# Performance work log

Hardware: AMD Instinct MI355X
Metric: run time of the kernel (lower is better)

Reference implementation:

```python
import jax, jax.numpy as jnp
import numpy as np

ALPHA = 1.0

def setup_inputs() -> dict:
    key = jax.random.key(0)
    kz, kc = jax.random.split(key)
    N, K, D = 65536, 256, 256
    z = jax.random.normal(kz, (N, D), dtype=jnp.float32)
    centroids = jax.random.normal(kc, (K, D), dtype=jnp.float32)
    return {"z": z, "centroids": centroids}

def reference(z, centroids):
    # squared euclidean distances (N, K) via expansion; same math as
    # sum((z[:,None,:]-c)**2, -1) without the (N,K,D) intermediate
    z2 = jnp.sum(z * z, axis=1, keepdims=True)            # (N, 1)
    c2 = jnp.sum(centroids * centroids, axis=1)           # (K,)
    sse = jnp.maximum(z2 + c2[None, :] - 2.0 * (z @ centroids.T), 0.0)
    # Student-t kernel
    q = (1.0 + sse / ALPHA) ** (-(ALPHA + 1.0) / 2.0)
    q = q / jnp.sum(q, axis=1, keepdims=True)             # row normalize
    # target distribution p
    sf = q * q / jnp.sum(q, axis=0, keepdims=True)        # col normalize of q^2
    p = sf / jnp.sum(sf, axis=1, keepdims=True)           # row normalize
    return (p, q)
```

## Files before the change

### kernel.cpp

```cpp
#include <hip/hip_runtime.h>
#include <stdint.h>

#define N_ROWS 65536
#define K_CENT 256
#define D_DIM  256

typedef __attribute__((ext_vector_type(8))) short bf16x8;
typedef __attribute__((ext_vector_type(4))) float f32x4;

__device__ __forceinline__ float bf2f(unsigned short u) {
    union { unsigned int i; float f; } v;
    v.i = ((unsigned int)u) << 16;
    return v.f;
}

__device__ __forceinline__ unsigned short f2bf(float f) {
    union { float f; unsigned int i; } v;
    v.f = f;
    unsigned int r = (v.i + 0x7FFFu + ((v.i >> 16) & 1u)) >> 16;
    return (unsigned short)r;
}

__global__ void c2_kernel(const float* __restrict__ cent,
                          float* __restrict__ c2,
                          unsigned short* __restrict__ cent_bf) {
    int row  = blockIdx.x;
    int lane = threadIdx.x;
    const float4 v = *(const float4*)(cent + (size_t)row * D_DIM + lane * 4);
    unsigned short b0 = f2bf(v.x), b1 = f2bf(v.y), b2 = f2bf(v.z), b3 = f2bf(v.w);
    ushort4 bv; bv.x = b0; bv.y = b1; bv.z = b2; bv.w = b3;
    *(ushort4*)(cent_bf + (size_t)row * D_DIM + lane * 4) = bv;
    float f0 = bf2f(b0), f1 = bf2f(b1), f2 = bf2f(b2), f3 = bf2f(b3);
    float s = f0 * f0 + f1 * f1 + f2 * f2 + f3 * f3;
    #pragma unroll
    for (int off = 32; off >= 1; off >>= 1) s += __shfl_xor(s, off, 64);
    if (lane == 0) c2[row] = s;
}

__global__ void pass1_kernel(const float* __restrict__ z,
                             const unsigned short* __restrict__ cent_bf,
                             const float* __restrict__ c2,
                             float* __restrict__ s_col,
                             float* __restrict__ q_out) {
    __shared__ float col_lds[4][K_CENT];

    const int tid  = threadIdx.x;
    const int wave = tid >> 6;
    const int lane = tid & 63;
    const int m15  = lane & 15;
    const int quad = lane >> 4;
    const int row0 = blockIdx.x * 64 + wave * 16;

    f32x4 acc[16];
    #pragma unroll
    for (int t = 0; t < 16; ++t) acc[t] = (f32x4){0.f, 0.f, 0.f, 0.f};

    const float*          za = z + (size_t)(row0 + m15) * D_DIM + quad * 8;
    const unsigned short* ba = cent_bf + (size_t)m15 * D_DIM + quad * 8;

    float z2p = 0.0f;
    for (int ks = 0; ks < D_DIM; ks += 32) {
        float4 a0 = *(const float4*)(za + ks);
        float4 a1 = *(const float4*)(za + ks + 4);
        bf16x8 afrag;
        unsigned short ub[8];
        ub[0] = f2bf(a0.x); ub[1] = f2bf(a0.y); ub[2] = f2bf(a0.z); ub[3] = f2bf(a0.w);
        ub[4] = f2bf(a1.x); ub[5] = f2bf(a1.y); ub[6] = f2bf(a1.z); ub[7] = f2bf(a1.w);
        #pragma unroll
        for (int j = 0; j < 8; ++j) {
            afrag[j] = (short)ub[j];
            float f = bf2f(ub[j]);
            z2p += f * f;
        }
        #pragma unroll
        for (int t = 0; t < 16; ++t) {
            bf16x8 bfrag = *(const bf16x8*)(ba + (size_t)t * 16 * D_DIM + ks);
            acc[t] = __builtin_amdgcn_mfma_f32_16x16x32_bf16(afrag, bfrag, acc[t], 0, 0, 0);
        }
    }

    z2p += __shfl_xor(z2p, 16, 64);
    z2p += __shfl_xor(z2p, 32, 64);
    float z2r[4];
    #pragma unroll
    for (int r = 0; r < 4; ++r) z2r[r] = __shfl(z2p, quad * 4 + r, 64);

    float rowsum[4] = {0.f, 0.f, 0.f, 0.f};
    #pragma unroll
    for (int t = 0; t < 16; ++t) {
        float c2v = c2[t * 16 + m15];
        #pragma unroll
        for (int r = 0; r < 4; ++r) {
            float sse = z2r[r] + c2v - 2.0f * acc[t][r];
            sse = fmaxf(sse, 0.0f);
            float u = 1.0f / (1.0f + sse);
            acc[t][r] = u;
            rowsum[r] += u;
        }
    }
    #pragma unroll
    for (int r = 0; r < 4; ++r) {
        float v = rowsum[r];
        v += __shfl_xor(v, 1, 64);
        v += __shfl_xor(v, 2, 64);
        v += __shfl_xor(v, 4, 64);
        v += __shfl_xor(v, 8, 64);
        rowsum[r] = 1.0f / v;
    }

    float colp[16];
    #pragma unroll
    for (int t = 0; t < 16; ++t) {
        float cp = 0.0f;
        #pragma unroll
        for (int r = 0; r < 4; ++r) {
            float qv = acc[t][r] * rowsum[r];
            cp += qv;
            q_out[(size_t)(row0 + quad * 4 + r) * K_CENT + t * 16 + m15] = qv;
        }
        cp += __shfl_xor(cp, 16, 64);
        cp += __shfl_xor(cp, 32, 64);
        colp[t] = cp;
    }
    if (quad == 0) {
        #pragma unroll
        for (int t = 0; t < 16; ++t) col_lds[wave][t * 16 + lane] = colp[t];
    }
    __syncthreads();
    float sp = col_lds[0][tid] + col_lds[1][tid] + col_lds[2][tid] + col_lds[3][tid];
    atomicAdd(&s_col[tid], sp);
}

__global__ void pass2_kernel(const float* __restrict__ q,
                             const float* __restrict__ s_col,
                             float* __restrict__ p) {
    const int tid  = threadIdx.x;
    const int lane = tid & 63;
    const int wave = tid >> 6;
    const int wid  = blockIdx.x * 4 + wave;

    const float4 sv = *(const float4*)(s_col + lane * 4);
    const float is0 = 1.0f / sv.x, is1 = 1.0f / sv.y,
                is2 = 1.0f / sv.z, is3 = 1.0f / sv.w;

    for (int it = 0; it < 32; ++it) {
        const int row = wid * 32 + it;
        const float4 qv = *(const float4*)(q + (size_t)row * K_CENT + lane * 4);
        float sf0 = qv.x * qv.x * is0, sf1 = qv.y * qv.y * is1;
        float sf2 = qv.z * qv.z * is2, sf3 = qv.w * qv.w * is3;
        float part = sf0 + sf1 + sf2 + sf3;
        #pragma unroll
        for (int off = 32; off >= 1; off >>= 1) part += __shfl_xor(part, off, 64);
        const float rinv = 1.0f / part;
        float4 ov;
        ov.x = sf0 * rinv; ov.y = sf1 * rinv;
        ov.z = sf2 * rinv; ov.w = sf3 * rinv;
        *(float4*)(p + (size_t)row * K_CENT + lane * 4) = ov;
    }
}

extern "C" void kernel_launch(void* const* d_in, const int* in_sizes, int n_in,
                              void* d_out, int out_size, void* d_ws, size_t ws_size,
                              hipStream_t stream) {
    const float* z    = (const float*)d_in[0];
    const float* cent = (const float*)d_in[1];
    float* p_out = (float*)d_out;
    float* q_out = p_out + (size_t)N_ROWS * K_CENT;

    float* c2    = (float*)d_ws;
    float* s_col = c2 + K_CENT;
    unsigned short* cent_bf = (unsigned short*)(s_col + K_CENT);

    hipMemsetAsync(s_col, 0, K_CENT * sizeof(float), stream);
    c2_kernel<<<K_CENT, 64, 0, stream>>>(cent, c2, cent_bf);
    pass1_kernel<<<N_ROWS / 64, 256, 0, stream>>>(z, cent_bf, c2, s_col, q_out);
    pass2_kernel<<<N_ROWS / (4 * 32), 256, 0, stream>>>(q_out, s_col, p_out);
}
```

Baseline: 256.6 us.

## Stage swizzled bf16 centroids in LDS and preload A fragments; widen pass2 grid

Pass1 loads all A fragments (z rows converted to bf16) into registers first. It then streams the bf16 centroids through a 32KB LDS buffer in four 64-row chunks, using an XOR swizzle written by c2_kernel so the B-fragment reads avoid bank conflicts. Previously every wave read B fragments straight from global/L2. Pass2 now handles 8 rows per wave with all loads issued up front, giving four times as many blocks and more memory-level parallelism. The costs are extra syncthreads, LDS use that limits occupancy, and higher register pressure.

Measured after the change: 230.4 us. 1.11x faster.

```diff
diff --git a/kernel.cpp b/kernel.cpp
--- a/kernel.cpp
+++ b/kernel.cpp
@@ -29,7 +29,9 @@
     const float4 v = *(const float4*)(cent + (size_t)row * D_DIM + lane * 4);
     unsigned short b0 = f2bf(v.x), b1 = f2bf(v.y), b2 = f2bf(v.z), b3 = f2bf(v.w);
     ushort4 bv; bv.x = b0; bv.y = b1; bv.z = b2; bv.w = b3;
-    *(ushort4*)(cent_bf + (size_t)row * D_DIM + lane * 4) = bv;
+    int blk = lane >> 1;
+    int pos = row * D_DIM + (((blk ^ (row & 7)) << 3) | ((lane & 1) << 2));
+    *(ushort4*)(cent_bf + pos) = bv;
     float f0 = bf2f(b0), f1 = bf2f(b1), f2 = bf2f(b2), f3 = bf2f(b3);
     float s = f0 * f0 + f1 * f1 + f2 * f2 + f3 * f3;
     #pragma unroll
@@ -37,11 +39,13 @@
     if (lane == 0) c2[row] = s;
 }
 
-__global__ void pass1_kernel(const float* __restrict__ z,
-                             const unsigned short* __restrict__ cent_bf,
-                             const float* __restrict__ c2,
-                             float* __restrict__ s_col,
-                             float* __restrict__ q_out) {
+__global__ __launch_bounds__(256, 4) void pass1_kernel(
+        const float* __restrict__ z,
+        const unsigned short* __restrict__ cent_bf,
+        const float* __restrict__ c2,
+        float* __restrict__ s_col,
+        float* __restrict__ q_out) {
+    __shared__ __align__(16) unsigned short bstage[64 * D_DIM];
     __shared__ float col_lds[4][K_CENT];
 
     const int tid  = threadIdx.x;
@@ -51,39 +55,55 @@
     const int quad = lane >> 4;
     const int row0 = blockIdx.x * 64 + wave * 16;
 
-    f32x4 acc[16];
-    #pragma unroll
-    for (int t = 0; t < 16; ++t) acc[t] = (f32x4){0.f, 0.f, 0.f, 0.f};
-
-    const float*          za = z + (size_t)(row0 + m15) * D_DIM + quad * 8;
-    const unsigned short* ba = cent_bf + (size_t)m15 * D_DIM + quad * 8;
-
+    const float* za = z + (size_t)(row0 + m15) * D_DIM + quad * 8;
+    bf16x8 afrag[8];
     float z2p = 0.0f;
-    for (int ks = 0; ks < D_DIM; ks += 32) {
-        float4 a0 = *(const float4*)(za + ks);
-        float4 a1 = *(const float4*)(za + ks + 4);
-        bf16x8 afrag;
-        unsigned short ub[8];
-        ub[0] = f2bf(a0.x); ub[1] = f2bf(a0.y); ub[2] = f2bf(a0.z); ub[3] = f2bf(a0.w);
-        ub[4] = f2bf(a1.x); ub[5] = f2bf(a1.y); ub[6] = f2bf(a1.z); ub[7] = f2bf(a1.w);
+    #pragma unroll
+    for (int ks = 0; ks < 8; ++ks) {
+        float4 a0 = *(const float4*)(za + ks * 32);
+        float4 a1 = *(const float4*)(za + ks * 32 + 4);
+        float av[8] = {a0.x, a0.y, a0.z, a0.w, a1.x, a1.y, a1.z, a1.w};
         #pragma unroll
         for (int j = 0; j < 8; ++j) {
-            afrag[j] = (short)ub[j];
-            float f = bf2f(ub[j]);
+            unsigned short ub = f2bf(av[j]);
+            afrag[ks][j] = (short)ub;
+            float f = bf2f(ub);
             z2p += f * f;
         }
-        #pragma unroll
-        for (int t = 0; t < 16; ++t) {
-            bf16x8 bfrag = *(const bf16x8*)(ba + (size_t)t * 16 * D_DIM + ks);
-            acc[t] = __builtin_amdgcn_mfma_f32_16x16x32_bf16(afrag, bfrag, acc[t], 0, 0, 0);
-        }
-    }
-
+    }
     z2p += __shfl_xor(z2p, 16, 64);
     z2p += __shfl_xor(z2p, 32, 64);
     float z2r[4];
     #pragma unroll
     for (int r = 0; r < 4; ++r) z2r[r] = __shfl(z2p, quad * 4 + r, 64);
+
+    f32x4 acc[16];
+    #pragma unroll
+    for (int t = 0; t < 16; ++t) acc[t] = (f32x4){0.f, 0.f, 0.f, 0.f};
+
+    #pragma unroll
+    for (int c = 0; c < 4; ++c) {
+        const unsigned short* src = cent_bf + (size_t)c * 64 * D_DIM;
+        #pragma unroll
+        for (int i = 0; i < 8; ++i) {
+            int off = (i * 256 + tid) * 8;
+            *(bf16x8*)&bstage[off] = *(const bf16x8*)&src[off];
+        }
+        __syncthreads();
+        #pragma unroll
+        for (int ks = 0; ks < 8; ++ks) {
+            #pragma unroll
+            for (int t = 0; t < 4; ++t) {
+                int r_local = t * 16 + m15;
+                int b = quad + ks * 4;
+                int pos = r_local * D_DIM + ((b ^ (r_local & 7)) << 3);
+                bf16x8 bfrag = *(const bf16x8*)&bstage[pos];
+                acc[c * 4 + t] = __builtin_amdgcn_mfma_f32_16x16x32_bf16(
+                    afrag[ks], bfrag, acc[c * 4 + t], 0, 0, 0);
+            }
+        }
+        __syncthreads();
+    }
 
     float rowsum[4] = {0.f, 0.f, 0.f, 0.f};
     #pragma unroll
@@ -131,9 +151,10 @@
     atomicAdd(&s_col[tid], sp);
 }
 
-__global__ void pass2_kernel(const float* __restrict__ q,
-                             const float* __restrict__ s_col,
-                             float* __restrict__ p) {
+__global__ __launch_bounds__(256) void pass2_kernel(
+        const float* __restrict__ q,
+        const float* __restrict__ s_col,
+        float* __restrict__ p) {
     const int tid  = threadIdx.x;
     const int lane = tid & 63;
     const int wave = tid >> 6;
@@ -143,11 +164,19 @@
     const float is0 = 1.0f / sv.x, is1 = 1.0f / sv.y,
                 is2 = 1.0f / sv.z, is3 = 1.0f / sv.w;
 
-    for (int it = 0; it < 32; ++it) {
-        const int row = wid * 32 + it;
-        const float4 qv = *(const float4*)(q + (size_t)row * K_CENT + lane * 4);
-        float sf0 = qv.x * qv.x * is0, sf1 = qv.y * qv.y * is1;
-        float sf2 = qv.z * qv.z * is2, sf3 = qv.w * qv.w * is3;
+    const float* qb = q + (size_t)wid * 8 * K_CENT + lane * 4;
+    float*       pb = p + (size_t)wid * 8 * K_CENT + lane * 4;
+
+    float4 qv[8];
+    #pragma unroll
+    for (int r = 0; r < 8; ++r) qv[r] = *(const float4*)(qb + r * K_CENT);
+
+    #pragma unroll
+    for (int r = 0; r < 8; ++r) {
+        float sf0 = qv[r].x * qv[r].x * is0;
+        float sf1 = qv[r].y * qv[r].y * is1;
+        float sf2 = qv[r].z * qv[r].z * is2;
+        float sf3 = qv[r].w * qv[r].w * is3;
         float part = sf0 + sf1 + sf2 + sf3;
         #pragma unroll
         for (int off = 32; off >= 1; off >>= 1) part += __shfl_xor(part, off, 64);
@@ -155,7 +184,7 @@
         float4 ov;
         ov.x = sf0 * rinv; ov.y = sf1 * rinv;
         ov.z = sf2 * rinv; ov.w = sf3 * rinv;
-        *(float4*)(p + (size_t)row * K_CENT + lane * 4) = ov;
+        *(float4*)(pb + r * K_CENT) = ov;
     }
 }
 
@@ -174,5 +203,5 @@
     hipMemsetAsync(s_col, 0, K_CENT * sizeof(float), stream);
     c2_kernel<<<K_CENT, 64, 0, stream>>>(cent, c2, cent_bf);
     pass1_kernel<<<N_ROWS / 64, 256, 0, stream>>>(z, cent_bf, c2, s_col, q_out);
-    pass2_kernel<<<N_ROWS / (4 * 32), 256, 0, stream>>>(q_out, s_col, p_out);
-}
+    pass2_kernel<<<N_ROWS / (4 * 8), 256, 0, stream>>>(q_out, s_col, p_out);
+}
```
